# Kernel optimization log

Hardware: AMD Instinct MI355X
Metric: run time of the kernel (lower is better)

Reference implementation:

```python
import jax, jax.numpy as jnp
import numpy as np

B, T, C = 2, 2048, 2048
NH, G, HS = 16, 4, 128          # heads, kv groups, head dim
QPK = NH // G                    # queries per kv group
K = 4                            # conv kernel width
WIN = 512                        # sliding window (local_window)
SCALE = 1.0 / np.sqrt(HS)


def causal_conv1d_silu(x, w):
    # x: [B, T, D] channels-last, w: [D, K] depthwise kernel; causal left-pad then SiLU
    xp = jnp.pad(x, ((0, 0), (K - 1, 0), (0, 0)))
    out = sum(w[None, None, :, k] * xp[:, k:k + T, :] for k in range(K))
    return jax.nn.silu(out)


def apply_rope(x, cos, sin):
    # x: [B, T, H, HS], cos/sin: [T, HS//2]; non-interleaved halves rotation
    d = cos.shape[-1]
    x1, x2 = x[..., :d], x[..., d:]
    c = cos[None, :, None, :]
    s = sin[None, :, None, :]
    return jnp.concatenate([x1 * c - x2 * s, x1 * s + x2 * c], axis=-1)


def setup_inputs() -> dict:
    key = jax.random.key(0)
    ks = jax.random.split(key, 6)
    x = jax.random.normal(ks[0], (B, T, C), jnp.float32)
    Wqkv = jax.random.normal(ks[1], (C, (NH + 2 * G) * HS), jnp.float32) * 0.02
    Wproj = jax.random.normal(ks[2], (NH * HS, C), jnp.float32) * 0.02
    q_conv_w = jax.random.normal(ks[3], (NH * HS, K), jnp.float32) * 0.3
    k_conv_w = jax.random.normal(ks[4], (G * HS, K), jnp.float32) * 0.3
    v_conv_w = jax.random.normal(ks[5], (G * HS, K), jnp.float32) * 0.3
    # RoPE cache as in build_rope_cache
    theta = 1.0 / (10000.0 ** (jnp.arange(0, HS, 2, dtype=jnp.float32) / HS))
    idx = jnp.outer(jnp.arange(T, dtype=jnp.float32), theta)  # [T, HS//2]
    cos, sin = jnp.cos(idx), jnp.sin(idx)
    return {"x": x, "Wqkv": Wqkv, "Wproj": Wproj,
            "q_conv_w": q_conv_w, "k_conv_w": k_conv_w, "v_conv_w": v_conv_w,
            "cos": cos, "sin": sin}


def reference(x, Wqkv, Wproj, q_conv_w, k_conv_w, v_conv_w, cos, sin):
    # QKV projection + GQA split (group-major head layout, matches torch view/split)
    qkv = (x @ Wqkv).reshape(B, T, G, QPK + 2, HS)
    q = qkv[..., :QPK, :].reshape(B, T, NH * HS)
    k = qkv[..., QPK:QPK + 1, :].reshape(B, T, G * HS)
    v = qkv[..., QPK + 1:, :].reshape(B, T, G * HS)
    # short causal depthwise conv + silu on q/k/v
    q = causal_conv1d_silu(q, q_conv_w).reshape(B, T, NH, HS)
    k = causal_conv1d_silu(k, k_conv_w).reshape(B, T, G, HS)
    v = causal_conv1d_silu(v, v_conv_w).reshape(B, T, G, HS)
    # RoPE
    q = apply_rope(q, cos, sin)
    k = apply_rope(k, cos, sin)
    # expand kv groups to full heads (consecutive repeat matches group-major q)
    k = jnp.repeat(k, QPK, axis=2)  # [B, T, NH, HS]
    v = jnp.repeat(v, QPK, axis=2)
    # sliding-window causal attention
    scores = jnp.einsum('bthd,bshd->bhts', q, k) * SCALE  # [B, NH, T, T]
    i = jnp.arange(T)[:, None]
    j = jnp.arange(T)[None, :]
    mask = (j <= i) & (i - j < WIN)
    scores = jnp.where(mask, scores, jnp.finfo(scores.dtype).min)
    p = jax.nn.softmax(scores, axis=-1)
    y = jnp.einsum('bhts,bshd->bthd', p, v).reshape(B, T, NH * HS)
    return y @ Wproj
```

## Files before the change

### kernel.cpp

```cpp
#include <hip/hip_runtime.h>
#include <math.h>
#include <stdint.h>

#define B_    2
#define T_    2048
#define C_    2048
#define NH_   16
#define G_    4
#define HS_   128
#define WIN_  512
#define NQKV_ 3072
#define M_    4096
#define SCALE_ 0.08838834764831845f

typedef __attribute__((ext_vector_type(8))) __bf16 bf16x8;
typedef __attribute__((ext_vector_type(4))) float f32x4;
typedef unsigned short u16;

static __device__ __forceinline__ u16 f2bf(float f) {
  union { float f; unsigned u; } v; v.f = f;
  unsigned r = v.u + 0x7fffu + ((v.u >> 16) & 1u);
  return (u16)(r >> 16);
}
static __device__ __forceinline__ float bf2f(u16 h) {
  union { unsigned u; float f; } v; v.u = ((unsigned)h) << 16; return v.f;
}
static __device__ __forceinline__ bf16x8 ldg8(const u16* p) {
  return *(const bf16x8*)(const void*)p;
}

__global__ void cvt_bf16(const float* __restrict__ in, u16* __restrict__ out) {
  int i = blockIdx.x * 256 + threadIdx.x;
  float4 v = ((const float4*)in)[i];
  ushort4 o;
  o.x = f2bf(v.x); o.y = f2bf(v.y); o.z = f2bf(v.z); o.w = f2bf(v.w);
  ((ushort4*)out)[i] = o;
}

__global__ void transpose_cvt(const float* __restrict__ in, u16* __restrict__ out,
                              int R, int Ccols) {
  __shared__ float tile[32][33];
  int c0 = blockIdx.x * 32, r0 = blockIdx.y * 32;
  int tx = threadIdx.x & 31, ty = threadIdx.x >> 5;
#pragma unroll
  for (int i = 0; i < 32; i += 8)
    tile[ty + i][tx] = in[(size_t)(r0 + ty + i) * Ccols + c0 + tx];
  __syncthreads();
#pragma unroll
  for (int i = 0; i < 32; i += 8)
    out[(size_t)(c0 + ty + i) * R + r0 + tx] = f2bf(tile[tx][ty + i]);
}

__global__ void transpose_v16(const u16* __restrict__ in, u16* __restrict__ out) {
  __shared__ u16 tile[32][33];
  int b = blockIdx.z;
  int c0 = blockIdx.x * 32, t0 = blockIdx.y * 32;
  int tx = threadIdx.x & 31, ty = threadIdx.x >> 5;
  const u16* src = in + (size_t)b * T_ * (G_*HS_);
  u16* dst = out + (size_t)b * (G_*HS_) * T_;
#pragma unroll
  for (int i = 0; i < 32; i += 8)
    tile[ty + i][tx] = src[(size_t)(t0 + ty + i) * (G_*HS_) + c0 + tx];
  __syncthreads();
#pragma unroll
  for (int i = 0; i < 32; i += 8)
    dst[(size_t)(c0 + ty + i) * T_ + t0 + tx] = tile[tx][ty + i];
}

template<int N, int K, int OUTBF>
__global__ __launch_bounds__(256)
void gemm_bt(const u16* __restrict__ A, const u16* __restrict__ Bt,
             u16* __restrict__ Cb, float* __restrict__ Cf) {
  __shared__ u16 lA[128 * 32];
  __shared__ u16 lB[128 * 32];
  const int m0 = blockIdx.x * 128;
  const int n0 = blockIdx.y * 128;
  const int lane = threadIdx.x & 63;
  const int wave = threadIdx.x >> 6;
  const int wr = (wave >> 1) * 64, wc = (wave & 1) * 64;
  const int fr = lane & 15, fk = (lane >> 4) * 8;
  const int srow = lane >> 2;
  const int scol = (lane & 3) * 8;
  f32x4 acc[4][4] = {};
  for (int k0 = 0; k0 < K; k0 += 32) {
#pragma unroll
    for (int c = 0; c < 2; ++c) {
      int chunk = wave * 2 + c;
      int row = chunk * 16 + srow;
      __builtin_amdgcn_global_load_lds(
          (__attribute__((address_space(1))) void*)(A + (size_t)(m0 + row) * K + k0 + scol),
          (__attribute__((address_space(3))) void*)(lA + chunk * 512), 16, 0, 0);
      __builtin_amdgcn_global_load_lds(
          (__attribute__((address_space(1))) void*)(Bt + (size_t)(n0 + row) * K + k0 + scol),
          (__attribute__((address_space(3))) void*)(lB + chunk * 512), 16, 0, 0);
    }
    __syncthreads();
    bf16x8 af[4], bb[4];
#pragma unroll
    for (int i = 0; i < 4; ++i) {
      af[i] = ldg8(lA + (wr + i * 16 + fr) * 32 + fk);
      bb[i] = ldg8(lB + (wc + i * 16 + fr) * 32 + fk);
    }
#pragma unroll
    for (int i = 0; i < 4; ++i)
#pragma unroll
      for (int j = 0; j < 4; ++j)
        acc[i][j] = __builtin_amdgcn_mfma_f32_16x16x32_bf16(af[i], bb[j], acc[i][j], 0, 0, 0);
    __syncthreads();
  }
  const int orow = m0 + wr + (lane >> 4) * 4;
  const int ocol = n0 + wc + fr;
#pragma unroll
  for (int i = 0; i < 4; ++i)
#pragma unroll
    for (int j = 0; j < 4; ++j)
#pragma unroll
      for (int jj = 0; jj < 4; ++jj) {
        int r = orow + i * 16 + jj, cc = ocol + j * 16;
        if (OUTBF) Cb[(size_t)r * N + cc] = f2bf(acc[i][j][jj]);
        else       Cf[(size_t)r * N + cc] = acc[i][j][jj];
      }
}

__global__ void conv_rope_q(const u16* __restrict__ qkv, const float* __restrict__ w,
                            const float* __restrict__ cosT, const float* __restrict__ sinT,
                            u16* __restrict__ qout) {
  int tid = blockIdx.x * 256 + threadIdx.x;
  int d8 = (tid & 7) << 3;
  int h  = (tid >> 3) & 15;
  int bt = tid >> 7;
  int t  = bt & (T_ - 1);
  int g = h >> 2, s = h & 3;
  int col = (g * 6 + s) * 128 + d8;
  const u16* p = qkv + (size_t)bt * NQKV_ + col;

  bf16x8 lo[4], hi[4];
  const bf16x8 z8 = {};
#pragma unroll
  for (int k = 0; k < 4; ++k) {
    if (t + k >= 3) {
      long off = (long)(k - 3) * NQKV_;
      lo[k] = ldg8(p + off);
      hi[k] = ldg8(p + off + 64);
    } else { lo[k] = z8; hi[k] = z8; }
  }
  float4 c0 = *(const float4*)(cosT + t * 64 + d8);
  float4 c1 = *(const float4*)(cosT + t * 64 + d8 + 4);
  float4 s0 = *(const float4*)(sinT + t * 64 + d8);
  float4 s1 = *(const float4*)(sinT + t * 64 + d8 + 4);
  float cv[8] = {c0.x, c0.y, c0.z, c0.w, c1.x, c1.y, c1.z, c1.w};
  float sv[8] = {s0.x, s0.y, s0.z, s0.w, s1.x, s1.y, s1.z, s1.w};

  union { u16 a[8]; bf16x8 v; } olo, ohi;
#pragma unroll
  for (int j = 0; j < 8; ++j) {
    float4 wl = *(const float4*)(w + (size_t)(h * 128 + d8 + j) * 4);
    float4 wh = *(const float4*)(w + (size_t)(h * 128 + 64 + d8 + j) * 4);
    float a1 = wl.x * (float)lo[0][j] + wl.y * (float)lo[1][j] +
               wl.z * (float)lo[2][j] + wl.w * (float)lo[3][j];
    float a2 = wh.x * (float)hi[0][j] + wh.y * (float)hi[1][j] +
               wh.z * (float)hi[2][j] + wh.w * (float)hi[3][j];
    a1 = a1 / (1.f + __expf(-a1));
    a2 = a2 / (1.f + __expf(-a2));
    olo.a[j] = f2bf((a1 * cv[j] - a2 * sv[j]) * SCALE_);
    ohi.a[j] = f2bf((a1 * sv[j] + a2 * cv[j]) * SCALE_);
  }
  u16* dst = qout + ((size_t)bt * NH_ + h) * HS_ + d8;
  *(bf16x8*)(dst) = olo.v;
  *(bf16x8*)(dst + 64) = ohi.v;
}

__global__ void conv_kv(const u16* __restrict__ qkv, const float* __restrict__ kw,
                        const float* __restrict__ vw, const float* __restrict__ cosT,
                        const float* __restrict__ sinT,
                        u16* __restrict__ kout, u16* __restrict__ vtmp) {
  int tid = blockIdx.x * 256 + threadIdx.x;
  int idx = tid & 63;
  int bt  = tid >> 6;
  int t   = bt & (T_ - 1);
  int isv = idx >> 5;
  int g   = (idx >> 3) & 3;
  int d8  = (idx & 7) << 3;
  int col = (g * 6 + 4 + isv) * 128 + d8;
  const float* w = isv ? vw : kw;
  const u16* p = qkv + (size_t)bt * NQKV_ + col;

  bf16x8 lo[4], hi[4];
  const bf16x8 z8 = {};
#pragma unroll
  for (int k = 0; k < 4; ++k) {
    if (t + k >= 3) {
      long off = (long)(k - 3) * NQKV_;
      lo[k] = ldg8(p + off);
      hi[k] = ldg8(p + off + 64);
    } else { lo[k] = z8; hi[k] = z8; }
  }

  float a1[8], a2[8];
#pragma unroll
  for (int j = 0; j < 8; ++j) {
    float4 wl = *(const float4*)(w + (size_t)(g * 128 + d8 + j) * 4);
    float4 wh = *(const float4*)(w + (size_t)(g * 128 + 64 + d8 + j) * 4);
    float x1 = wl.x * (float)lo[0][j] + wl.y * (float)lo[1][j] +
               wl.z * (float)lo[2][j] + wl.w * (float)lo[3][j];
    float x2 = wh.x * (float)hi[0][j] + wh.y * (float)hi[1][j] +
               wh.z * (float)hi[2][j] + wh.w * (float)hi[3][j];
    a1[j] = x1 / (1.f + __expf(-x1));
    a2[j] = x2 / (1.f + __expf(-x2));
  }

  union { u16 a[8]; bf16x8 v; } olo, ohi;
  if (isv == 0) {
#pragma unroll
    for (int j = 0; j < 8; ++j) {
      float c = cosT[t * 64 + d8 + j], sn = sinT[t * 64 + d8 + j];
      olo.a[j] = f2bf(a1[j] * c - a2[j] * sn);
      ohi.a[j] = f2bf(a1[j] * sn + a2[j] * c);
    }
    u16* dst = kout + ((size_t)bt * G_ + g) * HS_ + d8;
    *(bf16x8*)(dst) = olo.v;
    *(bf16x8*)(dst + 64) = ohi.v;
  } else {
#pragma unroll
    for (int j = 0; j < 8; ++j) {
      olo.a[j] = f2bf(a1[j]);
      ohi.a[j] = f2bf(a2[j]);
    }
    u16* dst = vtmp + ((size_t)bt * G_ + g) * HS_ + d8;
    *(bf16x8*)(dst) = olo.v;
    *(bf16x8*)(dst + 64) = ohi.v;
  }
}

__global__ __launch_bounds__(256, 2)
void attn_swin(const u16* __restrict__ qbf, const u16* __restrict__ kbf,
               const u16* __restrict__ vt, u16* __restrict__ ybf) {
  __shared__ __align__(16) char kls[2][16384];
  __shared__ __align__(16) char vls[2][16384];
  __shared__ __align__(16) char pls[4][2048];
  const int lane = threadIdx.x & 63;
  const int wave = threadIdx.x >> 6;
  const int btile = blockIdx.x & 31;
  const int h  = (blockIdx.x >> 5) & 15;
  const int b  = blockIdx.x >> 9;
  const int g  = h >> 2;
  const int t0b = btile << 6;
  const int t0w = t0b + wave * 16;
  const int fr = lane & 15;
  const int hi = lane >> 4;
  const int fko = hi * 8;
  const int qr = t0w + fr;
  char* pl = pls[wave];
  const int swz = (fr & 7) << 4;

  const int krow_l = (lane >> 4);
  const int kcb    = (lane & 15) * 16;
  const int vrow_l = (lane >> 3);
  const int vcb    = (lane & 7) * 16;

  bf16x8 qf[4];
  {
    const u16* qb = qbf + ((size_t)((b * T_ + t0w + fr) * NH_ + h)) * HS_ + fko;
#pragma unroll
    for (int kc = 0; kc < 4; ++kc) qf[kc] = ldg8(qb + kc * 32);
  }

  int sbeg = t0b - (WIN_ - 1); if (sbeg < 0) sbeg = 0; sbeg &= ~63;
  const int nt = (t0b + 64 - sbeg) >> 6;

  const char* kgbase = (const char*)kbf + (((size_t)(b * T_) * G_ + g) * HS_) * 2;
  const char* vgbase = (const char*)vt + ((size_t)(b * (G_*HS_) + g * HS_)) * T_ * 2;

  auto stage = [&](int bufi, int s0) {
    char* kb = kls[bufi]; char* vb = vls[bufi];
#pragma unroll
    for (int c = 0; c < 4; ++c) {
      int i = wave * 4 + c;
      {
        int row = i * 4 + krow_l;
        int scb = kcb ^ ((row & 7) << 4);
        const char* src = kgbase + (size_t)(s0 + row) * (G_*HS_*2) + scb;
        __builtin_amdgcn_global_load_lds(
            (__attribute__((address_space(1))) void*)src,
            (__attribute__((address_space(3))) void*)(kb + i * 1024), 16, 0, 0);
      }
      {
        int row = i * 8 + vrow_l;
        int scb = vcb ^ ((row & 7) << 4);
        const char* src = vgbase + (size_t)row * (T_*2) + (size_t)s0 * 2 + scb;
        __builtin_amdgcn_global_load_lds(
            (__attribute__((address_space(1))) void*)src,
            (__attribute__((address_space(3))) void*)(vb + i * 1024), 16, 0, 0);
      }
    }
  };

  f32x4 acc_o[8];
#pragma unroll
  for (int n = 0; n < 8; ++n) acc_o[n] = (f32x4){0.f, 0.f, 0.f, 0.f};
  float m_r = -1e30f, l_r = 0.f;

  stage(0, sbeg);
  __syncthreads();
  int cur = 0;

  for (int t = 0; t < nt; ++t) {
    int s0 = sbeg + (t << 6);
    if (t + 1 < nt) stage(cur ^ 1, s0 + 64);
    const char* kb = kls[cur];
    const char* vb = vls[cur];

    f32x4 st[4];
    __builtin_amdgcn_s_setprio(1);
#pragma unroll
    for (int c = 0; c < 4; ++c) {
      st[c] = (f32x4){0.f, 0.f, 0.f, 0.f};
      int row = c * 16 + fr;
#pragma unroll
      for (int kc = 0; kc < 4; ++kc) {
        bf16x8 kf = *(const bf16x8*)(kb + row * 256 + ((kc * 64 + hi * 16) ^ swz));
        st[c] = __builtin_amdgcn_mfma_f32_16x16x32_bf16(kf, qf[kc], st[c], 0, 0, 0);
      }
    }
    __builtin_amdgcn_s_setprio(0);

    float tmax = -1e30f;
#pragma unroll
    for (int c = 0; c < 4; ++c)
#pragma unroll
      for (int j = 0; j < 4; ++j) {
        int key = s0 + c * 16 + hi * 4 + j;
        int dlt = qr - key;
        float x = (dlt >= 0 && dlt < WIN_) ? st[c][j] : -1e30f;
        st[c][j] = x;
        tmax = fmaxf(tmax, x);
      }
    tmax = fmaxf(tmax, __shfl_xor(tmax, 16, 64));
    tmax = fmaxf(tmax, __shfl_xor(tmax, 32, 64));
    float mn  = fmaxf(m_r, tmax);
    float fac = __expf(m_r - mn);
    m_r = mn;

    float ps = 0.f;
#pragma unroll
    for (int c = 0; c < 4; ++c) {
      union { ushort4 u4; __bf16 hh[4]; } pk;
#pragma unroll
      for (int j = 0; j < 4; ++j) {
        float p = (st[c][j] > -1e29f) ? __expf(st[c][j] - mn) : 0.f;
        ps += p;
        pk.hh[j] = (__bf16)p;
      }
      *(ushort4*)(pl + fr * 128 + ((c * 32 + hi * 8) ^ swz)) = pk.u4;
    }
    ps += __shfl_xor(ps, 16, 64);
    ps += __shfl_xor(ps, 32, 64);
    l_r = l_r * fac + ps;

    float fq0 = __shfl(fac, hi * 4 + 0, 64);
    float fq1 = __shfl(fac, hi * 4 + 1, 64);
    float fq2 = __shfl(fac, hi * 4 + 2, 64);
    float fq3 = __shfl(fac, hi * 4 + 3, 64);
#pragma unroll
    for (int n = 0; n < 8; ++n) {
      acc_o[n][0] *= fq0; acc_o[n][1] *= fq1;
      acc_o[n][2] *= fq2; acc_o[n][3] *= fq3;
    }

#pragma unroll
    for (int ch = 0; ch < 2; ++ch) {
      bf16x8 pa = *(const bf16x8*)(pl + fr * 128 + ((ch * 64 + hi * 16) ^ swz));
      __builtin_amdgcn_s_setprio(1);
#pragma unroll
      for (int n = 0; n < 8; ++n) {
        int row = n * 16 + fr;
        bf16x8 vf = *(const bf16x8*)(vb + row * 128 + ((ch * 64 + hi * 16) ^ swz));
        acc_o[n] = __builtin_amdgcn_mfma_f32_16x16x32_bf16(pa, vf, acc_o[n], 0, 0, 0);
      }
      __builtin_amdgcn_s_setprio(0);
    }
    __syncthreads();
    cur ^= 1;
  }

  float inv = 1.f / l_r;
  float iq[4];
#pragma unroll
  for (int j = 0; j < 4; ++j) iq[j] = __shfl(inv, hi * 4 + j, 64);
#pragma unroll
  for (int n = 0; n < 8; ++n)
#pragma unroll
    for (int jj = 0; jj < 4; ++jj) {
      int t = t0w + hi * 4 + jj;
      ybf[((size_t)(b * T_ + t)) * (NH_*HS_) + h * HS_ + n * 16 + fr] = f2bf(acc_o[n][jj] * iq[jj]);
    }
}

extern "C" void kernel_launch(void* const* d_in, const int* in_sizes, int n_in,
                              void* d_out, int out_size, void* d_ws, size_t ws_size,
                              hipStream_t stream) {
  (void)in_sizes; (void)n_in; (void)out_size;
  const float* x     = (const float*)d_in[0];
  const float* Wqkv  = (const float*)d_in[1];
  const float* Wproj = (const float*)d_in[2];
  const float* qw    = (const float*)d_in[3];
  const float* kw    = (const float*)d_in[4];
  const float* vw    = (const float*)d_in[5];
  const float* cosT  = (const float*)d_in[6];
  const float* sinT  = (const float*)d_in[7];
  float* out = (float*)d_out;
  char* ws = (char*)d_ws;

  u16* x_bf    = (u16*)(ws + 0);
  u16* wqkv_t  = (u16*)(ws + 16777216);
  u16* wproj_t = (u16*)(ws + 29360128);
  u16* qkv_bf  = (u16*)(ws + 37748736);
  u16* q_bf    = (u16*)(ws + 62914560);
  u16* k_bf    = (u16*)(ws + 79691776);
  u16* v_tmp   = (u16*)(ws + 83886080);
  u16* v_t     = (u16*)(ws + 88080384);
  u16* y_bf    = (u16*)(ws + 92274688);
  if (ws_size < (size_t)109051904) return;

  cvt_bf16<<<8192, 256, 0, stream>>>(x, x_bf);
  transpose_cvt<<<dim3(96, 64), 256, 0, stream>>>(Wqkv, wqkv_t, 2048, 3072);
  transpose_cvt<<<dim3(64, 64), 256, 0, stream>>>(Wproj, wproj_t, 2048, 2048);
  gemm_bt<3072, 2048, 1><<<dim3(32, 24), 256, 0, stream>>>(x_bf, wqkv_t, qkv_bf, nullptr);
  conv_rope_q<<<2048, 256, 0, stream>>>(qkv_bf, qw, cosT, sinT, q_bf);
  conv_kv<<<1024, 256, 0, stream>>>(qkv_bf, kw, vw, cosT, sinT, k_bf, v_tmp);
  transpose_v16<<<dim3(16, 64, 2), 256, 0, stream>>>(v_tmp, v_t);
  attn_swin<<<1024, 256, 0, stream>>>(q_bf, k_bf, v_t, y_bf);
  gemm_bt<2048, 2048, 0><<<dim3(32, 16), 256, 0, stream>>>(y_bf, wproj_t, nullptr, out);
}
```

Measured before the change: 213.5 us.

## Fuse prep and conv launches, double attention query tile, add lazy softmax rescale

Merges the x conversion and both weight transposes into one launch, and the q and kv conv kernels into another, to cut launch overhead. The attention kernel now gives each wave 32 query rows instead of 16, so every K/V tile staged in LDS feeds twice as many MFMAs. This halves the grid to 512 blocks and raises register pressure. It also skips the running-max update and output rescale when the new max stays within a threshold of the old one, which trades some numerical headroom for fewer exp and multiply operations.

After: 204.2 us, median of 2. 4.4% less time.

```diff
diff --git a/kernel.cpp b/kernel.cpp
--- a/kernel.cpp
+++ b/kernel.cpp
@@ -29,18 +29,31 @@
   return *(const bf16x8*)(const void*)p;
 }
 
-__global__ void cvt_bf16(const float* __restrict__ in, u16* __restrict__ out) {
-  int i = blockIdx.x * 256 + threadIdx.x;
-  float4 v = ((const float4*)in)[i];
-  ushort4 o;
-  o.x = f2bf(v.x); o.y = f2bf(v.y); o.z = f2bf(v.z); o.w = f2bf(v.w);
-  ((ushort4*)out)[i] = o;
-}
-
-__global__ void transpose_cvt(const float* __restrict__ in, u16* __restrict__ out,
-                              int R, int Ccols) {
+__global__ void prep_all(const float* __restrict__ x, const float* __restrict__ Wqkv,
+                         const float* __restrict__ Wproj,
+                         u16* __restrict__ x_bf, u16* __restrict__ wqkv_t,
+                         u16* __restrict__ wproj_t) {
+  int blk = blockIdx.x;
+  if (blk < 8192) {
+    int i = blk * 256 + threadIdx.x;
+    float4 v = ((const float4*)x)[i];
+    ushort4 o;
+    o.x = f2bf(v.x); o.y = f2bf(v.y); o.z = f2bf(v.z); o.w = f2bf(v.w);
+    ((ushort4*)x_bf)[i] = o;
+    return;
+  }
   __shared__ float tile[32][33];
-  int c0 = blockIdx.x * 32, r0 = blockIdx.y * 32;
+  const float* in; u16* out; int R, Ccols, bx, by;
+  if (blk < 8192 + 6144) {
+    int idx = blk - 8192;
+    in = Wqkv; out = wqkv_t; R = 2048; Ccols = 3072;
+    bx = idx % 96; by = idx / 96;
+  } else {
+    int idx = blk - 14336;
+    in = Wproj; out = wproj_t; R = 2048; Ccols = 2048;
+    bx = idx & 63; by = idx >> 6;
+  }
+  int c0 = bx * 32, r0 = by * 32;
   int tx = threadIdx.x & 31, ty = threadIdx.x >> 5;
 #pragma unroll
   for (int i = 0; i < 32; i += 8)
@@ -122,113 +135,102 @@
       }
 }
 
-__global__ void conv_rope_q(const u16* __restrict__ qkv, const float* __restrict__ w,
-                            const float* __restrict__ cosT, const float* __restrict__ sinT,
-                            u16* __restrict__ qout) {
-  int tid = blockIdx.x * 256 + threadIdx.x;
-  int d8 = (tid & 7) << 3;
-  int h  = (tid >> 3) & 15;
-  int bt = tid >> 7;
-  int t  = bt & (T_ - 1);
-  int g = h >> 2, s = h & 3;
-  int col = (g * 6 + s) * 128 + d8;
-  const u16* p = qkv + (size_t)bt * NQKV_ + col;
-
-  bf16x8 lo[4], hi[4];
+__global__ void conv_all(const u16* __restrict__ qkv, const float* __restrict__ qw,
+                         const float* __restrict__ kw, const float* __restrict__ vw,
+                         const float* __restrict__ cosT, const float* __restrict__ sinT,
+                         u16* __restrict__ qout, u16* __restrict__ kout,
+                         u16* __restrict__ vtmp) {
+  int blk = blockIdx.x;
   const bf16x8 z8 = {};
-#pragma unroll
-  for (int k = 0; k < 4; ++k) {
-    if (t + k >= 3) {
-      long off = (long)(k - 3) * NQKV_;
-      lo[k] = ldg8(p + off);
-      hi[k] = ldg8(p + off + 64);
-    } else { lo[k] = z8; hi[k] = z8; }
-  }
-  float4 c0 = *(const float4*)(cosT + t * 64 + d8);
-  float4 c1 = *(const float4*)(cosT + t * 64 + d8 + 4);
-  float4 s0 = *(const float4*)(sinT + t * 64 + d8);
-  float4 s1 = *(const float4*)(sinT + t * 64 + d8 + 4);
-  float cv[8] = {c0.x, c0.y, c0.z, c0.w, c1.x, c1.y, c1.z, c1.w};
-  float sv[8] = {s0.x, s0.y, s0.z, s0.w, s1.x, s1.y, s1.z, s1.w};
-
-  union { u16 a[8]; bf16x8 v; } olo, ohi;
-#pragma unroll
-  for (int j = 0; j < 8; ++j) {
-    float4 wl = *(const float4*)(w + (size_t)(h * 128 + d8 + j) * 4);
-    float4 wh = *(const float4*)(w + (size_t)(h * 128 + 64 + d8 + j) * 4);
-    float a1 = wl.x * (float)lo[0][j] + wl.y * (float)lo[1][j] +
-               wl.z * (float)lo[2][j] + wl.w * (float)lo[3][j];
-    float a2 = wh.x * (float)hi[0][j] + wh.y * (float)hi[1][j] +
-               wh.z * (float)hi[2][j] + wh.w * (float)hi[3][j];
-    a1 = a1 / (1.f + __expf(-a1));
-    a2 = a2 / (1.f + __expf(-a2));
-    olo.a[j] = f2bf((a1 * cv[j] - a2 * sv[j]) * SCALE_);
-    ohi.a[j] = f2bf((a1 * sv[j] + a2 * cv[j]) * SCALE_);
-  }
-  u16* dst = qout + ((size_t)bt * NH_ + h) * HS_ + d8;
-  *(bf16x8*)(dst) = olo.v;
-  *(bf16x8*)(dst + 64) = ohi.v;
-}
-
-__global__ void conv_kv(const u16* __restrict__ qkv, const float* __restrict__ kw,
-                        const float* __restrict__ vw, const float* __restrict__ cosT,
-                        const float* __restrict__ sinT,
-                        u16* __restrict__ kout, u16* __restrict__ vtmp) {
-  int tid = blockIdx.x * 256 + threadIdx.x;
-  int idx = tid & 63;
-  int bt  = tid >> 6;
-  int t   = bt & (T_ - 1);
-  int isv = idx >> 5;
-  int g   = (idx >> 3) & 3;
-  int d8  = (idx & 7) << 3;
-  int col = (g * 6 + 4 + isv) * 128 + d8;
-  const float* w = isv ? vw : kw;
-  const u16* p = qkv + (size_t)bt * NQKV_ + col;
-
-  bf16x8 lo[4], hi[4];
-  const bf16x8 z8 = {};
-#pragma unroll
-  for (int k = 0; k < 4; ++k) {
-    if (t + k >= 3) {
-      long off = (long)(k - 3) * NQKV_;
-      lo[k] = ldg8(p + off);
-      hi[k] = ldg8(p + off + 64);
-    } else { lo[k] = z8; hi[k] = z8; }
-  }
-
-  float a1[8], a2[8];
-#pragma unroll
-  for (int j = 0; j < 8; ++j) {
-    float4 wl = *(const float4*)(w + (size_t)(g * 128 + d8 + j) * 4);
-    float4 wh = *(const float4*)(w + (size_t)(g * 128 + 64 + d8 + j) * 4);
-    float x1 = wl.x * (float)lo[0][j] + wl.y * (float)lo[1][j] +
-               wl.z * (float)lo[2][j] + wl.w * (float)lo[3][j];
-    float x2 = wh.x * (float)hi[0][j] + wh.y * (float)hi[1][j] +
-               wh.z * (float)hi[2][j] + wh.w * (float)hi[3][j];
-    a1[j] = x1 / (1.f + __expf(-x1));
-    a2[j] = x2 / (1.f + __expf(-x2));
-  }
-
-  union { u16 a[8]; bf16x8 v; } olo, ohi;
-  if (isv == 0) {
+  if (blk < 2048) {
+    int tid = blk * 256 + threadIdx.x;
+    int d8 = (tid & 7) << 3;
+    int h  = (tid >> 3) & 15;
+    int bt = tid >> 7;
+    int t  = bt & (T_ - 1);
+    int g = h >> 2, s = h & 3;
+    int col = (g * 6 + s) * 128 + d8;
+    const u16* p = qkv + (size_t)bt * NQKV_ + col;
+    bf16x8 lo[4], hi[4];
+#pragma unroll
+    for (int k = 0; k < 4; ++k) {
+      if (t + k >= 3) {
+        long off = (long)(k - 3) * NQKV_;
+        lo[k] = ldg8(p + off);
+        hi[k] = ldg8(p + off + 64);
+      } else { lo[k] = z8; hi[k] = z8; }
+    }
+    union { u16 a[8]; bf16x8 v; } olo, ohi;
 #pragma unroll
     for (int j = 0; j < 8; ++j) {
+      float4 wl = *(const float4*)(qw + (size_t)(h * 128 + d8 + j) * 4);
+      float4 wh = *(const float4*)(qw + (size_t)(h * 128 + 64 + d8 + j) * 4);
+      float a1 = wl.x * (float)lo[0][j] + wl.y * (float)lo[1][j] +
+                 wl.z * (float)lo[2][j] + wl.w * (float)lo[3][j];
+      float a2 = wh.x * (float)hi[0][j] + wh.y * (float)hi[1][j] +
+                 wh.z * (float)hi[2][j] + wh.w * (float)hi[3][j];
+      a1 = a1 / (1.f + __expf(-a1));
+      a2 = a2 / (1.f + __expf(-a2));
       float c = cosT[t * 64 + d8 + j], sn = sinT[t * 64 + d8 + j];
-      olo.a[j] = f2bf(a1[j] * c - a2[j] * sn);
-      ohi.a[j] = f2bf(a1[j] * sn + a2[j] * c);
-    }
-    u16* dst = kout + ((size_t)bt * G_ + g) * HS_ + d8;
+      olo.a[j] = f2bf((a1 * c - a2 * sn) * SCALE_);
+      ohi.a[j] = f2bf((a1 * sn + a2 * c) * SCALE_);
+    }
+    u16* dst = qout + ((size_t)bt * NH_ + h) * HS_ + d8;
     *(bf16x8*)(dst) = olo.v;
     *(bf16x8*)(dst + 64) = ohi.v;
   } else {
+    int tid = (blk - 2048) * 256 + threadIdx.x;
+    int idx = tid & 63;
+    int bt  = tid >> 6;
+    int t   = bt & (T_ - 1);
+    int isv = idx >> 5;
+    int g   = (idx >> 3) & 3;
+    int d8  = (idx & 7) << 3;
+    int col = (g * 6 + 4 + isv) * 128 + d8;
+    const float* w = isv ? vw : kw;
+    const u16* p = qkv + (size_t)bt * NQKV_ + col;
+    bf16x8 lo[4], hi[4];
+#pragma unroll
+    for (int k = 0; k < 4; ++k) {
+      if (t + k >= 3) {
+        long off = (long)(k - 3) * NQKV_;
+        lo[k] = ldg8(p + off);
+        hi[k] = ldg8(p + off + 64);
+      } else { lo[k] = z8; hi[k] = z8; }
+    }
+    float a1[8], a2[8];
 #pragma unroll
     for (int j = 0; j < 8; ++j) {
-      olo.a[j] = f2bf(a1[j]);
-      ohi.a[j] = f2bf(a2[j]);
-    }
-    u16* dst = vtmp + ((size_t)bt * G_ + g) * HS_ + d8;
-    *(bf16x8*)(dst) = olo.v;
-    *(bf16x8*)(dst + 64) = ohi.v;
+      float4 wl = *(const float4*)(w + (size_t)(g * 128 + d8 + j) * 4);
+      float4 wh = *(const float4*)(w + (size_t)(g * 128 + 64 + d8 + j) * 4);
+      float x1 = wl.x * (float)lo[0][j] + wl.y * (float)lo[1][j] +
+                 wl.z * (float)lo[2][j] + wl.w * (float)lo[3][j];
+      float x2 = wh.x * (float)hi[0][j] + wh.y * (float)hi[1][j] +
+                 wh.z * (float)hi[2][j] + wh.w * (float)hi[3][j];
+      a1[j] = x1 / (1.f + __expf(-x1));
+      a2[j] = x2 / (1.f + __expf(-x2));
+    }
+    union { u16 a[8]; bf16x8 v; } olo, ohi;
+    if (isv == 0) {
+#pragma unroll
+      for (int j = 0; j < 8; ++j) {
+        float c = cosT[t * 64 + d8 + j], sn = sinT[t * 64 + d8 + j];
+        olo.a[j] = f2bf(a1[j] * c - a2[j] * sn);
+        ohi.a[j] = f2bf(a1[j] * sn + a2[j] * c);
+      }
+      u16* dst = kout + ((size_t)bt * G_ + g) * HS_ + d8;
+      *(bf16x8*)(dst) = olo.v;
+      *(bf16x8*)(dst + 64) = ohi.v;
+    } else {
+#pragma unroll
+      for (int j = 0; j < 8; ++j) {
+        olo.a[j] = f2bf(a1[j]);
+        ohi.a[j] = f2bf(a2[j]);
+      }
+      u16* dst = vtmp + ((size_t)bt * G_ + g) * HS_ + d8;
+      *(bf16x8*)(dst) = olo.v;
+      *(bf16x8*)(dst + 64) = ohi.v;
+    }
   }
 }
 
@@ -237,19 +239,18 @@
                const u16* __restrict__ vt, u16* __restrict__ ybf) {
   __shared__ __align__(16) char kls[2][16384];
   __shared__ __align__(16) char vls[2][16384];
-  __shared__ __align__(16) char pls[4][2048];
+  __shared__ __align__(16) char pls[4][4096];
   const int lane = threadIdx.x & 63;
   const int wave = threadIdx.x >> 6;
-  const int btile = blockIdx.x & 31;
-  const int h  = (blockIdx.x >> 5) & 15;
-  const int b  = blockIdx.x >> 9;
+  const int btile = blockIdx.x & 15;
+  const int h  = (blockIdx.x >> 4) & 15;
+  const int b  = blockIdx.x >> 8;
   const int g  = h >> 2;
-  const int t0b = btile << 6;
-  const int t0w = t0b + wave * 16;
+  const int t0b = btile << 7;
+  const int t0w = t0b + wave * 32;
   const int fr = lane & 15;
   const int hi = lane >> 4;
   const int fko = hi * 8;
-  const int qr = t0w + fr;
   char* pl = pls[wave];
   const int swz = (fr & 7) << 4;
 
@@ -258,15 +259,16 @@
   const int vrow_l = (lane >> 3);
   const int vcb    = (lane & 7) * 16;
 
-  bf16x8 qf[4];
-  {
-    const u16* qb = qbf + ((size_t)((b * T_ + t0w + fr) * NH_ + h)) * HS_ + fko;
-#pragma unroll
-    for (int kc = 0; kc < 4; ++kc) qf[kc] = ldg8(qb + kc * 32);
+  bf16x8 qf[2][4];
+#pragma unroll
+  for (int qh = 0; qh < 2; ++qh) {
+    const u16* qb = qbf + ((size_t)((b * T_ + t0w + qh * 16 + fr) * NH_ + h)) * HS_ + fko;
+#pragma unroll
+    for (int kc = 0; kc < 4; ++kc) qf[qh][kc] = ldg8(qb + kc * 32);
   }
 
   int sbeg = t0b - (WIN_ - 1); if (sbeg < 0) sbeg = 0; sbeg &= ~63;
-  const int nt = (t0b + 64 - sbeg) >> 6;
+  const int nt = (t0b + 128 - sbeg) >> 6;
 
   const char* kgbase = (const char*)kbf + (((size_t)(b * T_) * G_ + g) * HS_) * 2;
   const char* vgbase = (const char*)vt + ((size_t)(b * (G_*HS_) + g * HS_)) * T_ * 2;
@@ -295,10 +297,12 @@
     }
   };
 
-  f32x4 acc_o[8];
-#pragma unroll
-  for (int n = 0; n < 8; ++n) acc_o[n] = (f32x4){0.f, 0.f, 0.f, 0.f};
-  float m_r = -1e30f, l_r = 0.f;
+  f32x4 acc_o[2][8];
+#pragma unroll
+  for (int qh = 0; qh < 2; ++qh)
+#pragma unroll
+    for (int n = 0; n < 8; ++n) acc_o[qh][n] = (f32x4){0.f, 0.f, 0.f, 0.f};
+  float m_r[2] = {-1e30f, -1e30f}, l_r[2] = {0.f, 0.f};
 
   stage(0, sbeg);
   __syncthreads();
@@ -310,72 +314,86 @@
     const char* kb = kls[cur];
     const char* vb = vls[cur];
 
-    f32x4 st[4];
+    f32x4 st[2][4];
+#pragma unroll
+    for (int qh = 0; qh < 2; ++qh)
+#pragma unroll
+      for (int c = 0; c < 4; ++c) st[qh][c] = (f32x4){0.f, 0.f, 0.f, 0.f};
     __builtin_amdgcn_s_setprio(1);
 #pragma unroll
     for (int c = 0; c < 4; ++c) {
-      st[c] = (f32x4){0.f, 0.f, 0.f, 0.f};
       int row = c * 16 + fr;
 #pragma unroll
       for (int kc = 0; kc < 4; ++kc) {
         bf16x8 kf = *(const bf16x8*)(kb + row * 256 + ((kc * 64 + hi * 16) ^ swz));
-        st[c] = __builtin_amdgcn_mfma_f32_16x16x32_bf16(kf, qf[kc], st[c], 0, 0, 0);
+        st[0][c] = __builtin_amdgcn_mfma_f32_16x16x32_bf16(kf, qf[0][kc], st[0][c], 0, 0, 0);
+        st[1][c] = __builtin_amdgcn_mfma_f32_16x16x32_bf16(kf, qf[1][kc], st[1][c], 0, 0, 0);
       }
     }
     __builtin_amdgcn_s_setprio(0);
 
-    float tmax = -1e30f;
-#pragma unroll
-    for (int c = 0; c < 4; ++c)
-#pragma unroll
-      for (int j = 0; j < 4; ++j) {
-        int key = s0 + c * 16 + hi * 4 + j;
-        int dlt = qr - key;
-        float x = (dlt >= 0 && dlt < WIN_) ? st[c][j] : -1e30f;
-        st[c][j] = x;
-        tmax = fmaxf(tmax, x);
-      }
-    tmax = fmaxf(tmax, __shfl_xor(tmax, 16, 64));
-    tmax = fmaxf(tmax, __shfl_xor(tmax, 32, 64));
-    float mn  = fmaxf(m_r, tmax);
-    float fac = __expf(m_r - mn);
-    m_r = mn;
-
-    float ps = 0.f;
-#pragma unroll
-    for (int c = 0; c < 4; ++c) {
-      union { ushort4 u4; __bf16 hh[4]; } pk;
-#pragma unroll
-      for (int j = 0; j < 4; ++j) {
-        float p = (st[c][j] > -1e29f) ? __expf(st[c][j] - mn) : 0.f;
-        ps += p;
-        pk.hh[j] = (__bf16)p;
-      }
-      *(ushort4*)(pl + fr * 128 + ((c * 32 + hi * 8) ^ swz)) = pk.u4;
-    }
-    ps += __shfl_xor(ps, 16, 64);
-    ps += __shfl_xor(ps, 32, 64);
-    l_r = l_r * fac + ps;
-
-    float fq0 = __shfl(fac, hi * 4 + 0, 64);
-    float fq1 = __shfl(fac, hi * 4 + 1, 64);
-    float fq2 = __shfl(fac, hi * 4 + 2, 64);
-    float fq3 = __shfl(fac, hi * 4 + 3, 64);
-#pragma unroll
-    for (int n = 0; n < 8; ++n) {
-      acc_o[n][0] *= fq0; acc_o[n][1] *= fq1;
-      acc_o[n][2] *= fq2; acc_o[n][3] *= fq3;
+#pragma unroll
+    for (int qh = 0; qh < 2; ++qh) {
+      int qr = t0w + qh * 16 + fr;
+      float tmax = -1e30f;
+#pragma unroll
+      for (int c = 0; c < 4; ++c)
+#pragma unroll
+        for (int j = 0; j < 4; ++j) {
+          int key = s0 + c * 16 + hi * 4 + j;
+          int dlt = qr - key;
+          float x = (dlt >= 0 && dlt < WIN_) ? st[qh][c][j] : -1e30f;
+          st[qh][c][j] = x;
+          tmax = fmaxf(tmax, x);
+        }
+      tmax = fmaxf(tmax, __shfl_xor(tmax, 16, 64));
+      tmax = fmaxf(tmax, __shfl_xor(tmax, 32, 64));
+      float fac = 1.f;
+      bool need = !__all(tmax <= m_r[qh] + 8.f);
+      if (need) {
+        float mn = fmaxf(m_r[qh], tmax);
+        fac = __expf(m_r[qh] - mn);
+        m_r[qh] = mn;
+      }
+      float ps = 0.f;
+#pragma unroll
+      for (int c = 0; c < 4; ++c) {
+        union { ushort4 u4; __bf16 hh[4]; } pk;
+#pragma unroll
+        for (int j = 0; j < 4; ++j) {
+          float p = (st[qh][c][j] > -1e29f) ? __expf(st[qh][c][j] - m_r[qh]) : 0.f;
+          ps += p;
+          pk.hh[j] = (__bf16)p;
+        }
+        *(ushort4*)(pl + (qh * 16 + fr) * 128 + ((c * 32 + hi * 8) ^ swz)) = pk.u4;
+      }
+      ps += __shfl_xor(ps, 16, 64);
+      ps += __shfl_xor(ps, 32, 64);
+      l_r[qh] = l_r[qh] * fac + ps;
+      if (need) {
+        float fq0 = __shfl(fac, hi * 4 + 0, 64);
+        float fq1 = __shfl(fac, hi * 4 + 1, 64);
+        float fq2 = __shfl(fac, hi * 4 + 2, 64);
+        float fq3 = __shfl(fac, hi * 4 + 3, 64);
+#pragma unroll
+        for (int n = 0; n < 8; ++n) {
+          acc_o[qh][n][0] *= fq0; acc_o[qh][n][1] *= fq1;
+          acc_o[qh][n][2] *= fq2; acc_o[qh][n][3] *= fq3;
+        }
+      }
     }
 
 #pragma unroll
     for (int ch = 0; ch < 2; ++ch) {
-      bf16x8 pa = *(const bf16x8*)(pl + fr * 128 + ((ch * 64 + hi * 16) ^ swz));
+      bf16x8 pa0 = *(const bf16x8*)(pl + fr * 128 + ((ch * 64 + hi * 16) ^ swz));
+      bf16x8 pa1 = *(const bf16x8*)(pl + (16 + fr) * 128 + ((ch * 64 + hi * 16) ^ swz));
       __builtin_amdgcn_s_setprio(1);
 #pragma unroll
       for (int n = 0; n < 8; ++n) {
         int row = n * 16 + fr;
         bf16x8 vf = *(const bf16x8*)(vb + row * 128 + ((ch * 64 + hi * 16) ^ swz));
-        acc_o[n] = __builtin_amdgcn_mfma_f32_16x16x32_bf16(pa, vf, acc_o[n], 0, 0, 0);
+        acc_o[0][n] = __builtin_amdgcn_mfma_f32_16x16x32_bf16(pa0, vf, acc_o[0][n], 0, 0, 0);
+        acc_o[1][n] = __builtin_amdgcn_mfma_f32_16x16x32_bf16(pa1, vf, acc_o[1][n], 0, 0, 0);
       }
       __builtin_amdgcn_s_setprio(0);
     }
@@ -383,17 +401,21 @@
     cur ^= 1;
   }
 
-  float inv = 1.f / l_r;
-  float iq[4];
-#pragma unroll
-  for (int j = 0; j < 4; ++j) iq[j] = __shfl(inv, hi * 4 + j, 64);
-#pragma unroll
-  for (int n = 0; n < 8; ++n)
-#pragma unroll
-    for (int jj = 0; jj < 4; ++jj) {
-      int t = t0w + hi * 4 + jj;
-      ybf[((size_t)(b * T_ + t)) * (NH_*HS_) + h * HS_ + n * 16 + fr] = f2bf(acc_o[n][jj] * iq[jj]);
-    }
+#pragma unroll
+  for (int qh = 0; qh < 2; ++qh) {
+    float inv = 1.f / l_r[qh];
+    float iq[4];
+#pragma unroll
+    for (int j = 0; j < 4; ++j) iq[j] = __shfl(inv, hi * 4 + j, 64);
+#pragma unroll
+    for (int n = 0; n < 8; ++n)
+#pragma unroll
+      for (int jj = 0; jj < 4; ++jj) {
+        int t = t0w + qh * 16 + hi * 4 + jj;
+        ybf[((size_t)(b * T_ + t)) * (NH_*HS_) + h * HS_ + n * 16 + fr] =
+            f2bf(acc_o[qh][n][jj] * iq[jj]);
+      }
+  }
 }
 
 extern "C" void kernel_launch(void* const* d_in, const int* in_sizes, int n_in,
@@ -422,13 +444,10 @@
   u16* y_bf    = (u16*)(ws + 92274688);
   if (ws_size < (size_t)109051904) return;
 
-  cvt_bf16<<<8192, 256, 0, stream>>>(x, x_bf);
-  transpose_cvt<<<dim3(96, 64), 256, 0, stream>>>(Wqkv, wqkv_t, 2048, 3072);
-  transpose_cvt<<<dim3(64, 64), 256, 0, stream>>>(Wproj, wproj_t, 2048, 2048);
+  prep_all<<<18432, 256, 0, stream>>>(x, Wqkv, Wproj, x_bf, wqkv_t, wproj_t);
   gemm_bt<3072, 2048, 1><<<dim3(32, 24), 256, 0, stream>>>(x_bf, wqkv_t, qkv_bf, nullptr);
-  conv_rope_q<<<2048, 256, 0, stream>>>(qkv_bf, qw, cosT, sinT, q_bf);
-  conv_kv<<<1024, 256, 0, stream>>>(qkv_bf, kw, vw, cosT, sinT, k_bf, v_tmp);
+  conv_all<<<3072, 256, 0, stream>>>(qkv_bf, qw, kw, vw, cosT, sinT, q_bf, k_bf, v_tmp);
   transpose_v16<<<dim3(16, 64, 2), 256, 0, stream>>>(v_tmp, v_t);
-  attn_swin<<<1024, 256, 0, stream>>>(q_bf, k_bf, v_t, y_bf);
+  attn_swin<<<512, 256, 0, stream>>>(q_bf, k_bf, v_t, y_bf);
   gemm_bt<2048, 2048, 0><<<dim3(32, 16), 256, 0, stream>>>(y_bf, wproj_t, nullptr, out);
 }
```
